# Performance work log

Hardware: AMD Instinct MI355X
Metric: run time of the kernel (lower is better)

Reference implementation:

```python
import jax, jax.numpy as jnp
import numpy as np

NEURON_CDECAY = 0.5
NEURON_VDECAY = 0.75
NEURON_VTH = 0.5
SPIKE_WINDOW = 0.5


@jax.custom_vjp
def pseudo_spike(v):
    return (v > NEURON_VTH).astype(v.dtype)

def _ps_fwd(v):
    return pseudo_spike(v), v

def _ps_bwd(v, g):
    return (g * (jnp.abs(v - NEURON_VTH) < SPIKE_WINDOW).astype(g.dtype),)

pseudo_spike.defvjp(_ps_fwd, _ps_bwd)


def setup_inputs() -> dict:
    key = jax.random.key(0)
    ks = jax.random.split(key, 6)
    B, S, T, H, A = 4096, 256, 50, 256, 2
    # NCP mask with fanout=256 over 256 targets selects every target -> dense.
    x = jax.random.uniform(ks[0], (B, S, T), dtype=jnp.float32)
    w1 = jax.random.normal(ks[1], (S, H), dtype=jnp.float32)
    w2 = jax.random.normal(ks[2], (H, H), dtype=jnp.float32)
    w3 = jax.random.normal(ks[3], (H, H), dtype=jnp.float32)
    w4 = jax.random.normal(ks[4], (H, A), dtype=jnp.float32)
    b1 = jnp.zeros((H,), jnp.float32)
    b2 = jnp.zeros((H,), jnp.float32)
    b3 = jnp.zeros((H,), jnp.float32)
    b4 = jnp.zeros((A,), jnp.float32)
    return {"x": x, "w1": w1, "b1": b1, "w2": w2, "b2": b2,
            "w3": w3, "b3": b3, "w4": w4, "b4": b4, "batch_size": B}


def _lif(pre, W, b, u, v, s):
    # torch: linear(pre, weight=W.t(), bias=b) == pre @ W + b  (W is [src, tgt])
    cur = u * NEURON_CDECAY + pre @ W + b
    volt = v * NEURON_VDECAY * (1.0 - s) + cur
    spk = pseudo_spike(volt)
    return cur, volt, spk


def reference(x, w1, b1, w2, b2, w3, b3, w4, b4, batch_size):
    B = x.shape[0]
    T = x.shape[2]
    H1, H2, H3, A = w1.shape[1], w2.shape[1], w3.shape[1], w4.shape[1]
    z = lambda d: jnp.zeros((B, d), x.dtype)
    carry0 = (z(H1), z(H1), z(H1), z(H2), z(H2), z(H2),
              z(H3), z(H3), z(H3), z(A), z(A), z(A))
    xt = jnp.transpose(x, (2, 0, 1))  # [T, B, S]

    def step(carry, inp):
        u1, v1, s1, u2, v2, s2, u3, v3, s3, u4, v4, s4 = carry
        u1, v1, s1 = _lif(inp, w1, b1, u1, v1, s1)
        u2, v2, s2 = _lif(s1, w2, b2, u2, v2, s2)
        u3, v3, s3 = _lif(s2, w3, b3, u3, v3, s3)
        u4, v4, s4 = _lif(s3, w4, b4, u4, v4, s4)
        return (u1, v1, s1, u2, v2, s2, u3, v3, s3, u4, v4, s4), s4

    _, s4_all = jax.lax.scan(step, carry0, xt)  # [T, B, A]
    fc4_sumspike = jnp.sum(s4_all, axis=0) / T
    # faithful to the source: out is divided by batch_window a second time
    out = fc4_sumspike / T
    return out
```

## Files before the change

kernel.cpp:

```cpp
#include <hip/hip_runtime.h>

typedef unsigned short u16;
typedef unsigned int u32;

#define B_N 4096
#define S_N 256
#define T_N 50
#define H_N 256

#define W1F 0
#define W2F 65536
#define W3F 131072
#define W4F 196608
#define B1F 197120
#define B2F 197376
#define B3F 197632
#define B4F 197888
#define CVT_N 197890
#define FLAGI 198656

__device__ __forceinline__ float bf2f(u16 h) { return __uint_as_float(((u32)h) << 16); }
__device__ __forceinline__ u16 f2bf(float f) {
  u32 x = __float_as_uint(f);
  return (u16)((x + 0x7fffu + ((x >> 16) & 1u)) >> 16);
}
__device__ __forceinline__ float ld_f(const void* p, size_t i, int isbf) {
  return isbf ? bf2f(((const u16*)p)[i]) : ((const float*)p)[i];
}

__global__ void detect_dtype(const u16* __restrict__ x, int* __restrict__ flag) {
  __shared__ int cnt[256];
  int c = 0;
  for (int i = threadIdx.x; i < 4096; i += 256) c += (x[2 * i] <= 0x3F80u) ? 1 : 0;
  cnt[threadIdx.x] = c;
  __syncthreads();
  if (threadIdx.x == 0) {
    int tot = 0;
    for (int i = 0; i < 256; i++) tot += cnt[i];
    flag[0] = (tot > 3000) ? 1 : 0;
  }
}

__global__ void convert_inputs(const void* w1, const void* w2, const void* w3,
                               const void* w4, const void* b1, const void* b2,
                               const void* b3, const void* b4, float* __restrict__ ws) {
  const int isbf = ((const int*)ws)[FLAGI];
  int i = blockIdx.x * 256 + threadIdx.x;
  if (i >= CVT_N) return;
  float v;
  if (i < 196608) {
    const void* src = (i < 65536) ? w1 : (i < 131072 ? w2 : w3);
    v = ld_f(src, (size_t)(i & 65535), isbf);
  } else if (i < 197120) v = ld_f(w4, (size_t)(i - W4F), isbf);
  else if (i < 197376) v = ld_f(b1, (size_t)(i - B1F), isbf);
  else if (i < 197632) v = ld_f(b2, (size_t)(i - B2F), isbf);
  else if (i < 197888) v = ld_f(b3, (size_t)(i - B3F), isbf);
  else v = ld_f(b4, (size_t)(i - B4F), isbf);
  ws[i] = v;
}

__global__ __launch_bounds__(256, 3) void snn_f32(
    const void* __restrict__ x, const float* __restrict__ ws, void* __restrict__ out) {
  __shared__ float Af[S_N][52];
  __shared__ float z4[T_N][2];

  const int b = blockIdx.x;
  const int tid = threadIdx.x;
  const int isbf = ((const int*)ws)[FLAGI];

  {
    const size_t base = ((size_t)b * S_N + tid) * T_N;
    if (isbf) {
      const u32* xr = (const u32*)((const u16*)x + base);
#pragma unroll
      for (int j = 0; j < 25; j++) {
        u32 d = xr[j];
        Af[tid][2 * j] = bf2f((u16)(d & 0xffffu));
        Af[tid][2 * j + 1] = bf2f((u16)(d >> 16));
      }
    } else {
      const float* xf = (const float*)x + base;
#pragma unroll
      for (int j = 0; j < 25; j++) {
        float2 d = *(const float2*)(xf + 2 * j);
        Af[tid][2 * j] = d.x;
        Af[tid][2 * j + 1] = d.y;
      }
    }
  }

  const int WOFF[3] = {W1F, W2F, W3F};
  const int BOFF[3] = {B1F, B2F, B3F};

  for (int l = 0; l < 3; l++) {
    __syncthreads();
    const float* W = ws + WOFF[l] + tid;

    float acc[T_N];
#pragma unroll
    for (int t = 0; t < T_N; t++) acc[t] = 0.0f;

    for (int s = 0; s < S_N; s++) {
      const float w = W[s << 8];
      const float4* ar = (const float4*)&Af[s][0];
      float4 av[12];
#pragma unroll
      for (int j = 0; j < 12; j++) av[j] = ar[j];
      float2 at = *(const float2*)&Af[s][48];
#pragma unroll
      for (int j = 0; j < 12; j++) {
        acc[4 * j + 0] = fmaf(av[j].x, w, acc[4 * j + 0]);
        acc[4 * j + 1] = fmaf(av[j].y, w, acc[4 * j + 1]);
        acc[4 * j + 2] = fmaf(av[j].z, w, acc[4 * j + 2]);
        acc[4 * j + 3] = fmaf(av[j].w, w, acc[4 * j + 3]);
      }
      acc[48] = fmaf(at.x, w, acc[48]);
      acc[49] = fmaf(at.y, w, acc[49]);
    }
    __syncthreads();

    {
      const float bh = ws[BOFF[l] + tid];
      float uu = 0.f, vv = 0.f, ss = 0.f;
#pragma unroll
      for (int t = 0; t < T_N; t++) {
        float cur = fmaf(uu, 0.5f, acc[t]) + bh;
        float t1 = vv * 0.75f;
        float volt = fmaf(t1, 1.0f - ss, cur);
        float sp = (volt > 0.5f) ? 1.0f : 0.0f;
        uu = cur; vv = volt; ss = sp;
        Af[tid][t] = sp;
      }
    }
  }

  __syncthreads();
  if (tid < 2 * T_N) {
    const int t = tid >> 1, a = tid & 1;
    float az = 0.f;
    const float* w4p = ws + W4F + a;
    for (int h = 0; h < H_N; h++) az = fmaf(Af[h][t], w4p[2 * h], az);
    z4[t][a] = az;
  }
  __syncthreads();
  if (tid < 2) {
    const float bh = ws[B4F + tid];
    float uu = 0.f, vv = 0.f, ss = 0.f, sum = 0.f;
    for (int t = 0; t < T_N; t++) {
      float cur = fmaf(uu, 0.5f, z4[t][tid]) + bh;
      float t1 = vv * 0.75f;
      float volt = fmaf(t1, 1.0f - ss, cur);
      float sp = (volt > 0.5f) ? 1.0f : 0.0f;
      uu = cur; vv = volt; ss = sp;
      sum += sp;
    }
    float o = sum / 50.0f / 50.0f;
    if (isbf) ((u16*)out)[b * 2 + tid] = f2bf(o);
    else ((float*)out)[b * 2 + tid] = o;
  }
}

extern "C" void kernel_launch(void* const* d_in, const int* in_sizes, int n_in,
                              void* d_out, int out_size, void* d_ws, size_t ws_size,
                              hipStream_t stream) {
  const void* x  = d_in[0];
  const void* w1 = d_in[1];
  const void* b1 = d_in[2];
  const void* w2 = d_in[3];
  const void* b2 = d_in[4];
  const void* w3 = d_in[5];
  const void* b3 = d_in[6];
  const void* w4 = d_in[7];
  const void* b4 = d_in[8];

  float* ws = (float*)d_ws;
  int* flag = (int*)d_ws + FLAGI;

  detect_dtype<<<1, 256, 0, stream>>>((const u16*)x, flag);
  convert_inputs<<<(CVT_N + 255) / 256, 256, 0, stream>>>(w1, w2, w3, w4, b1, b2, b3, b4, ws);
  snn_f32<<<B_N, 256, 0, stream>>>(x, ws, d_out);
}
```

Measured before the change: 1.420 ms.

## Retile layer GEMM into 4 hidden units by 13 timesteps per thread

Each thread now computes a 13x4 (timestep x hidden) tile instead of one hidden unit over all 50 timesteps. This cuts the shared-memory reads of the activation row per FMA, and each weight load is reused across 13 timesteps. The results go back through shared memory so the LIF recurrence can run per hidden unit, using vectorized reads and writes. This adds an extra shared-memory transpose step plus a barrier, and the three template branches diverge only per wavefront.

```diff
diff --git a/kernel.cpp b/kernel.cpp
--- a/kernel.cpp
+++ b/kernel.cpp
@@ -59,6 +59,29 @@
   ws[i] = v;
 }
 
+template <int OFF, int TN>
+__device__ __forceinline__ void gemm_win(const float* __restrict__ Wc,
+                                         const float (*__restrict__ A)[52],
+                                         int rdf, float (&acc)[13][4]) {
+  for (int s = 0; s < S_N; s++) {
+    const float w0 = Wc[(s << 8) + 0];
+    const float w1 = Wc[(s << 8) + 64];
+    const float w2 = Wc[(s << 8) + 128];
+    const float w3 = Wc[(s << 8) + 192];
+    const float4* ar = (const float4*)(&A[s][rdf]);
+    const float4 q0 = ar[0], q1 = ar[1], q2 = ar[2], q3 = ar[3];
+    const float a[16] = {q0.x, q0.y, q0.z, q0.w, q1.x, q1.y, q1.z, q1.w,
+                         q2.x, q2.y, q2.z, q2.w, q3.x, q3.y, q3.z, q3.w};
+#pragma unroll
+    for (int i = 0; i < TN; i++) {
+      acc[i][0] = fmaf(a[OFF + i], w0, acc[i][0]);
+      acc[i][1] = fmaf(a[OFF + i], w1, acc[i][1]);
+      acc[i][2] = fmaf(a[OFF + i], w2, acc[i][2]);
+      acc[i][3] = fmaf(a[OFF + i], w3, acc[i][3]);
+    }
+  }
+}
+
 __global__ __launch_bounds__(256, 3) void snn_f32(
     const void* __restrict__ x, const float* __restrict__ ws, void* __restrict__ out) {
   __shared__ float Af[S_N][52];
@@ -67,6 +90,11 @@
   const int b = blockIdx.x;
   const int tid = threadIdx.x;
   const int isbf = ((const int*)ws)[FLAGI];
+  const int tq = tid >> 6;
+  const int hp = tid & 63;
+  const int t0 = (tq < 2) ? 13 * tq : 26 + 12 * (tq - 2);
+  const int tn = (tq < 2) ? 13 : 12;
+  const int rdf = 12 * tq;
 
   {
     const size_t base = ((size_t)b * S_N + tid) * T_N;
@@ -94,42 +122,58 @@
 
   for (int l = 0; l < 3; l++) {
     __syncthreads();
-    const float* W = ws + WOFF[l] + tid;
-
-    float acc[T_N];
-#pragma unroll
-    for (int t = 0; t < T_N; t++) acc[t] = 0.0f;
-
-    for (int s = 0; s < S_N; s++) {
-      const float w = W[s << 8];
-      const float4* ar = (const float4*)&Af[s][0];
-      float4 av[12];
-#pragma unroll
-      for (int j = 0; j < 12; j++) av[j] = ar[j];
-      float2 at = *(const float2*)&Af[s][48];
-#pragma unroll
-      for (int j = 0; j < 12; j++) {
-        acc[4 * j + 0] = fmaf(av[j].x, w, acc[4 * j + 0]);
-        acc[4 * j + 1] = fmaf(av[j].y, w, acc[4 * j + 1]);
-        acc[4 * j + 2] = fmaf(av[j].z, w, acc[4 * j + 2]);
-        acc[4 * j + 3] = fmaf(av[j].w, w, acc[4 * j + 3]);
-      }
-      acc[48] = fmaf(at.x, w, acc[48]);
-      acc[49] = fmaf(at.y, w, acc[49]);
+    const float* Wc = ws + WOFF[l] + hp;
+
+    float acc[13][4];
+#pragma unroll
+    for (int i = 0; i < 13; i++) {
+#pragma unroll
+      for (int k = 0; k < 4; k++) acc[i][k] = 0.0f;
+    }
+
+    if (tq == 0)      gemm_win<0, 13>(Wc, Af, rdf, acc);
+    else if (tq == 1) gemm_win<1, 13>(Wc, Af, rdf, acc);
+    else              gemm_win<2, 12>(Wc, Af, rdf, acc);
+    __syncthreads();
+
+#pragma unroll
+    for (int i = 0; i < 13; i++) {
+      if (i < tn) {
+#pragma unroll
+        for (int k = 0; k < 4; k++) Af[hp + 64 * k][t0 + i] = acc[i][k];
+      }
     }
     __syncthreads();
 
     {
       const float bh = ws[BOFF[l] + tid];
+      float c[T_N];
+      {
+        const float4* rr = (const float4*)&Af[tid][0];
+#pragma unroll
+        for (int j = 0; j < 12; j++) {
+          float4 v = rr[j];
+          c[4 * j] = v.x; c[4 * j + 1] = v.y; c[4 * j + 2] = v.z; c[4 * j + 3] = v.w;
+        }
+        float2 v = *(const float2*)&Af[tid][48];
+        c[48] = v.x; c[49] = v.y;
+      }
       float uu = 0.f, vv = 0.f, ss = 0.f;
 #pragma unroll
       for (int t = 0; t < T_N; t++) {
-        float cur = fmaf(uu, 0.5f, acc[t]) + bh;
+        float cur = fmaf(uu, 0.5f, c[t]) + bh;
         float t1 = vv * 0.75f;
         float volt = fmaf(t1, 1.0f - ss, cur);
         float sp = (volt > 0.5f) ? 1.0f : 0.0f;
         uu = cur; vv = volt; ss = sp;
-        Af[tid][t] = sp;
+        c[t] = sp;
+      }
+      {
+        float4* wr = (float4*)&Af[tid][0];
+#pragma unroll
+        for (int j = 0; j < 12; j++)
+          wr[j] = make_float4(c[4 * j], c[4 * j + 1], c[4 * j + 2], c[4 * j + 3]);
+        *(float2*)&Af[tid][48] = make_float2(c[48], c[49]);
       }
     }
   }
```

Result: faster. 1.178 ms (-17.1%).
